# Kernel tuning notes

Hardware: AMD Instinct MI355X
Metric: run time of the kernel (lower is better)

The kernel has to match this reference:

```python
import jax, jax.numpy as jnp
import numpy as np
from jax import lax

DIM = 1024
H = 16          # num_heads
HD = DIM // H   # head dim (qk and v identical)
D_INNER = 4     # fast-weight inner dim
CHUNK = 16
BASE_LR = 1e-3
KSZ = 4         # short conv kernel size


def short_conv(x, w):
    # x: (b, l, c), w: (c, KSZ). Depthwise causal conv + residual (as in ShortConvolution).
    xT = jnp.transpose(x, (0, 2, 1))  # (b, c, l)
    y = lax.conv_general_dilated(xT, w[:, None, :], window_strides=(1,),
                                 padding=[(KSZ - 1, 0)], feature_group_count=x.shape[-1],
                                 dimension_numbers=('NCH', 'OIH', 'NCH'))
    return jnp.transpose(y + xT, (0, 2, 1))


def l2norm(x):
    # interpret torch.norm(..., dim=-1) as L2 normalization over head dim (required for shape consistency)
    return x / jnp.linalg.norm(x, axis=-1, keepdims=True)


def attn(q, k, v):
    # flash_attn_func equivalent: non-causal softmax attention, scale 1/sqrt(d)
    # q: (b, D, h, d), k/v: (b, L, h, d)
    s = jnp.einsum('bqhd,bkhd->bhqk', q, k) / jnp.sqrt(jnp.asarray(q.shape[-1], q.dtype))
    p = jax.nn.softmax(s, axis=-1)
    return jnp.einsum('bhqk,bkhd->bqhd', p, v)


def setup_inputs() -> dict:
    key = jax.random.key(0)
    ks = jax.random.split(key, 12)
    b, l = 4, 4096
    s = 1.0 / np.sqrt(DIM)
    return {
        'hidden_states': jax.random.normal(ks[0], (b, l, DIM), jnp.float32),
        'Wq': jax.random.normal(ks[1], (DIM, DIM), jnp.float32) * s,
        'Wk': jax.random.normal(ks[2], (DIM, DIM), jnp.float32) * s,
        'Wv': jax.random.normal(ks[3], (DIM, DIM), jnp.float32) * s,
        'Wlr': jax.random.normal(ks[4], (H * 2, DIM), jnp.float32) * s,
        'Wg': jax.random.normal(ks[5], (DIM, DIM), jnp.float32) * s,
        'Wo': jax.random.normal(ks[6], (DIM, DIM), jnp.float32) * s,
        'cq': jax.random.normal(ks[7], (DIM, KSZ), jnp.float32) * 0.1,
        'ck': jax.random.normal(ks[8], (DIM, KSZ), jnp.float32) * 0.1,
        'cv': jax.random.normal(ks[9], (DIM, KSZ), jnp.float32) * 0.1,
        'W_in_init': jax.random.normal(ks[10], (1, D_INNER, H, HD), jnp.float32) / np.sqrt(HD),
        'W_out_init': jax.random.normal(ks[11], (1, D_INNER, H, HD), jnp.float32) / np.sqrt(D_INNER),
        'ln_g': jnp.ones((HD,), jnp.float32),
        'ln_b': jnp.zeros((HD,), jnp.float32),
    }


def _forward(hidden_states, Wq, Wk, Wv, Wlr, Wg, Wo, cq, ck, cv, W_in_init, W_out_init, ln_g, ln_b):
    b, l, _ = hidden_states.shape
    q = l2norm(jax.nn.silu(short_conv(hidden_states @ Wq.T, cq)).reshape(b, l, H, HD))
    k = l2norm(jax.nn.silu(short_conv(hidden_states @ Wk.T, ck)).reshape(b, l, H, HD))
    v = jax.nn.silu(short_conv(hidden_states @ Wv.T, cv)).reshape(b, l, H, HD)
    lr = jax.nn.softplus(hidden_states @ Wlr.T + BASE_LR).reshape(b, l, H, 2)

    nc = l // CHUNK
    to_chunks = lambda x: x.reshape(b, nc, CHUNK, H, -1).transpose(1, 0, 2, 3, 4)
    qc, kc, vc, lrc = map(to_chunks, (q, k, v, lr))

    W_in0 = jnp.broadcast_to(W_in_init, (b, D_INNER, H, HD))
    W_out0 = jnp.broadcast_to(W_out_init, (b, D_INNER, H, HD))
    mask = jnp.tril(jnp.ones((CHUNK, CHUNK), jnp.float32))  # causal within chunk (diag kept)

    def step(carry, xs):
        W_in, W_out = carry
        q_t, k_t, v_t, lr_t = xs  # (b, CHUNK, H, d) / lr (b, CHUNK, H, 2)
        k_h = jax.nn.softmax(jnp.einsum('blhd,bDhd->blhD', k_t, W_in), axis=-1) * lr_t[..., 1:]
        q_h = jax.nn.softmax(jnp.einsum('blhd,bDhd->blhD', q_t, W_in), axis=-1)
        qk = jnp.einsum('bqhD,bkhD->bhqk', q_h, k_h) * mask
        o_t = jnp.einsum('bqhD,bDhd->bqhd', q_h, W_out) + jnp.einsum('bhqk,bkhd->bqhd', qk, v_t)
        W_out = W_out + jnp.einsum('bnhD,bnhd->bDhd', k_h, v_t)
        lr_in = lr_t[:, :1, :, 0:1]    # (b,1,h,1)
        lr_out = lr_t[:, :1, :, 1:2]
        # two nested test-time gradient steps via attention
        for _ in range(2):
            g_out = -attn(W_in, k_t, v_t)
            g_in = -attn(W_out, v_t, k_t)
            W_in = W_in - lr_in * g_in
            W_out = W_out - lr_out * g_out
        return (W_in, W_out), o_t

    _, o = lax.scan(step, (W_in0, W_out0), (qc, kc, vc, lrc))
    o = o.transpose(1, 0, 2, 3, 4).reshape(b, l, H, HD)

    mu = o.mean(-1, keepdims=True)
    var = ((o - mu) ** 2).mean(-1, keepdims=True)
    o = (o - mu) / jnp.sqrt(var + 1e-5) * ln_g + ln_b
    o = o.reshape(b, l, DIM)
    gate = hidden_states @ Wg.T
    return (o * gate) @ Wo.T


def reference(hidden_states, Wq, Wk, Wv, Wlr, Wg, Wo, cq, ck, cv, W_in_init, W_out_init, ln_g, ln_b):
    return _forward(hidden_states, Wq, Wk, Wv, Wlr, Wg, Wo, cq, ck, cv, W_in_init, W_out_init, ln_g, ln_b)
```

## Files before the change

### kernel.cpp

```cpp
#include <hip/hip_runtime.h>
#include <cstdint>
#include <cstddef>

#define DIM    1024
#define NH     16
#define HD     64
#define CHUNK_ 16
#define SEQ    4096
#define BATCH  4
#define NROWS  (BATCH * SEQ)
#define NCHUNK (SEQ / CHUNK_)
#define SEG    64
#define NSEG   (SEQ / SEG)

using bf16x8 = __attribute__((ext_vector_type(8))) short;
using f32x4  = __attribute__((ext_vector_type(4))) float;
typedef union { bf16x8 v; uint32_t u[4]; } B8;

#define MFMA16(a, b, c) __builtin_amdgcn_mfma_f32_16x16x32_bf16((a), (b), (c), 0, 0, 0)

__device__ __forceinline__ ushort f2bf(float f) {
    uint32_t u = __float_as_uint(f);
    u += 0x7FFFu + ((u >> 16) & 1u);
    return (ushort)(u >> 16);
}
__device__ __forceinline__ uint32_t pack2(float a, float b) {
    return (uint32_t)f2bf(a) | ((uint32_t)f2bf(b) << 16);
}
__device__ __forceinline__ float b2f(ushort u) {
    return __uint_as_float(((uint32_t)u) << 16);
}
__device__ __forceinline__ float dot4(const float4 a, const float4 b) {
    return a.x*b.x + a.y*b.y + a.z*b.z + a.w*b.w;
}

template <int N>
__device__ __forceinline__ float ror16(float x) {
    return __int_as_float(__builtin_amdgcn_update_dpp(
        0, __float_as_int(x), 0x120 + N, 0xF, 0xF, true));
}
__device__ __forceinline__ float dppsum16(float x) {
    x += ror16<1>(x); x += ror16<2>(x);
    x += ror16<4>(x); x += ror16<8>(x);
    return x;
}

#define SYNC() do { asm volatile("" ::: "memory");          \
                    __builtin_amdgcn_wave_barrier();        \
                    __builtin_amdgcn_sched_barrier(0); } while (0)

__device__ __forceinline__ void gl_lds16(const void* g, void* l) {
    __builtin_amdgcn_global_load_lds(
        (const __attribute__((address_space(1))) void*)g,
        (__attribute__((address_space(3))) void*)l, 16, 0, 0);
}

__global__ __launch_bounds__(256)
void f2b_kernel(const float* __restrict__ in, ushort* __restrict__ out, int n8)
{
    int i = blockIdx.x * 256 + threadIdx.x;
    const int stride = gridDim.x * 256;
    for (; i < n8; i += stride) {
        float4 a = *(const float4*)&in[(size_t)i * 8];
        float4 b = *(const float4*)&in[(size_t)i * 8 + 4];
        uint4 u;
        u.x = pack2(a.x, a.y); u.y = pack2(a.z, a.w);
        u.z = pack2(b.x, b.y); u.w = pack2(b.z, b.w);
        *(uint4*)&out[(size_t)i * 8] = u;
    }
}

#define GEMM_LDS_BODY(EPILOG)                                                  \
    __shared__ ushort As[128][64];                                             \
    __shared__ ushort Bs[128][64];                                             \
    const int tid  = threadIdx.x, wave = tid >> 6, lane = tid & 63;            \
    const int m0   = blockIdx.y * 128, n0 = blockIdx.x * 128;                  \
    const int lo   = lane & 15, kg = lane >> 4;                                \
    const int wm   = (wave >> 1) * 64, wn = (wave & 1) * 64;                   \
    const int rin  = lane >> 3, sl = lane & 7;                                 \
    const int sb   = 32 * wave;                                                \
    f32x4 acc[4][4];                                                           \
    _Pragma("unroll")                                                          \
    for (int i = 0; i < 4; ++i)                                                \
        _Pragma("unroll")                                                      \
        for (int j = 0; j < 4; ++j) acc[i][j] = (f32x4){0.f, 0.f, 0.f, 0.f};   \
    const int swz = lo & 7;                                                    \
    for (int kt = 0; kt < K; kt += 64) {                                       \
        __syncthreads();                                                       \
        _Pragma("unroll")                                                      \
        for (int i = 0; i < 4; ++i) {                                          \
            const int row = sb + 8 * i + rin;                                  \
            const int gs  = sl ^ (row & 7);                                    \
            gl_lds16(A + (size_t)(m0 + row) * K + kt + gs * 8,                 \
                     &As[sb + 8 * i][0]);                                      \
            gl_lds16(B + (size_t)(n0 + row) * K + kt + gs * 8,                 \
                     &Bs[sb + 8 * i][0]);                                      \
        }                                                                      \
        __syncthreads();                                                       \
        bf16x8 af[2][4], bfr[2][4];                                            \
        _Pragma("unroll")                                                      \
        for (int kk = 0; kk < 2; ++kk)                                         \
            _Pragma("unroll")                                                  \
            for (int m = 0; m < 4; ++m) {                                      \
                const int s = (kk * 4 + kg) ^ swz;                             \
                af[kk][m]  = *(const bf16x8*)&As[wm + m * 16 + lo][s * 8];     \
                bfr[kk][m] = *(const bf16x8*)&Bs[wn + m * 16 + lo][s * 8];     \
            }                                                                  \
        _Pragma("unroll")                                                      \
        for (int kk = 0; kk < 2; ++kk)                                         \
            _Pragma("unroll")                                                  \
            for (int mt = 0; mt < 4; ++mt)                                     \
                _Pragma("unroll")                                              \
                for (int nt = 0; nt < 4; ++nt)                                 \
                    acc[mt][nt] = MFMA16(af[kk][mt], bfr[kk][nt], acc[mt][nt]);\
    }                                                                          \
    const int col = lane & 15, r4 = (lane >> 4) * 4;                           \
    _Pragma("unroll")                                                          \
    for (int mt = 0; mt < 4; ++mt)                                             \
        _Pragma("unroll")                                                      \
        for (int nt = 0; nt < 4; ++nt)                                         \
            _Pragma("unroll")                                                  \
            for (int j = 0; j < 4; ++j) {                                      \
                size_t idx = (size_t)(m0 + wm + mt * 16 + r4 + j) * DIM +      \
                             n0 + wn + nt * 16 + col;                          \
                EPILOG;                                                        \
            }

__global__ __launch_bounds__(256)
void gemm_lds_b16o(const ushort* __restrict__ A, const ushort* __restrict__ B,
                   ushort* __restrict__ C, int K)
{
    GEMM_LDS_BODY(C[idx] = f2bf(acc[mt][nt][j]))
}

__global__ __launch_bounds__(256)
void gemm_lds_f32o(const ushort* __restrict__ A, const ushort* __restrict__ B,
                   float* __restrict__ C, int K)
{
    GEMM_LDS_BODY(C[idx] = acc[mt][nt][j])
}

__global__ __launch_bounds__(256)
void lr_kernel(const float* __restrict__ hs, const float* __restrict__ Wlr,
               float* __restrict__ LR)
{
    __shared__ float row[DIM];
    const int r = blockIdx.x;
    const int t = threadIdx.x;
    *(float4*)&row[t * 4] = *(const float4*)&hs[(size_t)r * DIM + t * 4];
    __syncthreads();

    const int o = t >> 3;
    const int p = t & 7;
    const float* w = Wlr + (size_t)o * DIM + p * 128;
    const float* x = row + p * 128;
    float acc = 0.f;
#pragma unroll
    for (int i = 0; i < 32; ++i) {
        float4 xv = *(const float4*)(x + i * 4);
        float4 wv = *(const float4*)(w + i * 4);
        acc += dot4(xv, wv);
    }
    acc += __shfl_xor(acc, 1);
    acc += __shfl_xor(acc, 2);
    acc += __shfl_xor(acc, 4);
    if (p == 0) {
        float xx = acc + 0.001f;
        LR[(size_t)r * 32 + o] = (xx > 20.f) ? xx : log1pf(expf(xx));
    }
}

__global__ __launch_bounds__(256)
void halo_save(const ushort* __restrict__ Q, const ushort* __restrict__ K,
               const ushort* __restrict__ V, ushort* __restrict__ HALO)
{
    int idx = blockIdx.x;
    int tn  = idx / (BATCH * (NSEG - 1) * 3);
    int rem = idx - tn * (BATCH * (NSEG - 1) * 3);
    int b   = rem / ((NSEG - 1) * 3);
    int rem2= rem - b * ((NSEG - 1) * 3);
    int s   = rem2 / 3 + 1;
    int j   = rem2 - (s - 1) * 3;

    const ushort* buf = (tn == 0) ? Q : ((tn == 1) ? K : V);
    size_t src = ((size_t)(b * SEQ + s * SEG - 3 + j)) * DIM + threadIdx.x * 4;
    size_t dst = ((size_t)((tn * BATCH + b) * NSEG + s) * 3 + j) * DIM + threadIdx.x * 4;
    *(uint2*)&HALO[dst] = *(const uint2*)&buf[src];
}

__global__ __launch_bounds__(256)
void conv_inplace(ushort* __restrict__ Q, ushort* __restrict__ K,
                  ushort* __restrict__ V, const ushort* __restrict__ HALO,
                  const float* __restrict__ cq, const float* __restrict__ ck,
                  const float* __restrict__ cv)
{
    const int wid  = (blockIdx.x << 2) + (threadIdx.x >> 6);
    const int lane = threadIdx.x & 63;
    const int tn   = wid >> 12;
    const int rem  = wid & 4095;
    const int b    = rem >> 10;
    const int rem2 = rem & 1023;
    const int h    = rem2 >> 6;
    const int s    = rem2 & 63;
    const int c    = (h << 6) + lane;

    ushort* buf = (tn == 0) ? Q : ((tn == 1) ? K : V);
    const float* cw = (tn == 0) ? cq : ((tn == 1) ? ck : cv);
    float4 w4 = *(const float4*)(cw + (c << 2));

    float xm3 = 0.f, xm2 = 0.f, xm1 = 0.f;
    if (s > 0) {
        size_t hb = ((size_t)((tn * BATCH + b) * NSEG + s) * 3) * DIM + c;
        xm3 = b2f(HALO[hb]);
        xm2 = b2f(HALO[hb + DIM]);
        xm1 = b2f(HALO[hb + 2 * DIM]);
    }

    size_t base = ((size_t)(b * SEQ + s * SEG)) * DIM + c;
    float x_next = b2f(buf[base]);
#pragma unroll 4
    for (int i = 0; i < SEG; ++i) {
        float x = x_next;
        if (i < SEG - 1) x_next = b2f(buf[base + (size_t)(i + 1) * DIM]);
        float y = xm3 * w4.x + xm2 * w4.y + xm1 * w4.z + x * w4.w + x;
        y = y / (1.f + __expf(-y));
        if (tn < 2) {
            float n2 = y * y;
#pragma unroll
            for (int m = 1; m < 64; m <<= 1) n2 += __shfl_xor(n2, m);
            y *= rsqrtf(n2);
        }
        buf[base + (size_t)i * DIM] = f2bf(y);
        xm3 = xm2; xm2 = xm1; xm1 = x;
    }
}

__global__ __launch_bounds__(64)
void scan_kernel(const ushort* QP, const ushort* __restrict__ KP,
                 const ushort* __restrict__ VP, const float* __restrict__ LRb,
                 const float* __restrict__ GATE,
                 const float* __restrict__ Wi0, const float* __restrict__ Wo0,
                 const float* __restrict__ lng, const float* __restrict__ lnb,
                 ushort* OB)
{
    const int bh = blockIdx.x, b = bh >> 4, h = bh & 15;
    const int t  = threadIdx.x, lo = t & 15, g = t >> 4;

    __shared__ ushort KA2[2][16][72], QA2[2][16][72], VA2[2][16][72];
    __shared__ float  sG2[2][16][68];
    __shared__ ushort KT2[2][64][24];
    __shared__ ushort VT2[2][64][40];
    __shared__ ushort WiA[16][72], WoA[16][72];
    __shared__ ushort QKT[16][32], KH[16][32];

    for (int i = t; i < 16 * 72; i += 64) { ((ushort*)WiA)[i] = 0; ((ushort*)WoA)[i] = 0; }
    for (int i = t; i < 2 * 64 * 24; i += 64) ((ushort*)KT2)[i] = 0;
    for (int i = t; i < 2 * 64 * 40; i += 64) ((ushort*)VT2)[i] = 0;
    for (int i = t; i < 16 * 32; i += 64) { ((ushort*)QKT)[i] = 0; ((ushort*)KH)[i] = 0; }

    f32x4 wiC[4], woC[4];
#pragma unroll
    for (int n = 0; n < 4; ++n) { wiC[n] = (f32x4){0,0,0,0}; woC[n] = (f32x4){0,0,0,0}; }
    if (g == 0) {
#pragma unroll
        for (int n = 0; n < 4; ++n)
#pragma unroll
            for (int D = 0; D < 4; ++D) {
                float wi = Wi0[((size_t)D * NH + h) * HD + 16 * n + lo];
                float wo = Wo0[((size_t)D * NH + h) * HD + 16 * n + lo];
                wiC[n][D] = wi; woC[n][D] = wo;
                WiA[D][16 * n + lo] = f2bf(wi);
                WoA[D][16 * n + lo] = f2bf(wo);
                VT2[0][16 * n + lo][16 + D] = f2bf(wo);
            }
    }
    SYNC();

    float lnGr[4], lnBr[4];
#pragma unroll
    for (int n = 0; n < 4; ++n) { lnGr[n] = lng[16 * n + lo]; lnBr[n] = lnb[16 * n + lo]; }

    const int rowb = b * SEQ;
    const ushort* QPh = QP + h * 64;
    const ushort* KPh = KP + h * 64;
    const ushort* VPh = VP + h * 64;
    const float*  GPh = GATE + h * 64;
    ushort*       OBh = OB + h * 64;

    uint2 pq[4], pk[4], pv[4];
    float4 pg[4];
    float plr_q, plr_i, plr_o;

    {
#pragma unroll
        for (int i = 0; i < 4; ++i) {
            size_t go = (size_t)(rowb + i * 4 + g) * DIM + 4 * lo;
            pq[i] = *(const uint2*)&QPh[go];
            pk[i] = *(const uint2*)&KPh[go];
            pv[i] = *(const uint2*)&VPh[go];
            pg[i] = *(const float4*)&GPh[go];
        }
        plr_q = LRb[(size_t)(rowb + lo) * 32 + h * 2 + 1];
        plr_i = LRb[(size_t)rowb * 32 + h * 2];
        plr_o = LRb[(size_t)rowb * 32 + h * 2 + 1];
    }

    auto STAGE = [&](int nb) {
#pragma unroll
        for (int i = 0; i < 4; ++i) {
            const int row = i * 4 + g;
            *(float4*)&sG2[nb][row][4 * lo] = pg[i];
            *(uint2*)&QA2[nb][row][4 * lo] = pq[i];
            *(uint2*)&KA2[nb][row][4 * lo] = pk[i];
            *(uint2*)&VA2[nb][row][4 * lo] = pv[i];
            uint2 uk = pk[i], uv = pv[i];
            KT2[nb][4 * lo + 0][row] = (ushort)(uk.x & 0xFFFF);
            KT2[nb][4 * lo + 1][row] = (ushort)(uk.x >> 16);
            KT2[nb][4 * lo + 2][row] = (ushort)(uk.y & 0xFFFF);
            KT2[nb][4 * lo + 3][row] = (ushort)(uk.y >> 16);
            VT2[nb][4 * lo + 0][row] = (ushort)(uv.x & 0xFFFF);
            VT2[nb][4 * lo + 1][row] = (ushort)(uv.x >> 16);
            VT2[nb][4 * lo + 2][row] = (ushort)(uv.y & 0xFFFF);
            VT2[nb][4 * lo + 3][row] = (ushort)(uv.y >> 16);
        }
    };

    STAGE(0);
    SYNC();

    const f32x4 z4 = (f32x4){0.f, 0.f, 0.f, 0.f};
    const uint32_t pmsk = (g < 2) ? 0xFFFFFFFFu : 0u;
    const int L0 = (lo + 32 * g) & 63, L1 = (L0 + 16) & 63;

    for (int c = 0; c < NCHUNK; ++c) {
        const int rb  = rowb + c * CHUNK_;
        const int cur = c & 1, nxt = cur ^ 1;
        ushort (*KAc)[72] = KA2[cur];
        ushort (*QAc)[72] = QA2[cur];
        ushort (*VAc)[72] = VA2[cur];
        float  (*sGc)[68] = sG2[cur];
        ushort (*KTc)[24] = KT2[cur];
        ushort (*VTc)[40] = VT2[cur];

        const float lr1    = plr_q;
        const float lr_in  = plr_i;
        const float lr_out = plr_o;

        if (c + 1 < NCHUNK) {
            const int rb2 = rb + CHUNK_;
#pragma unroll
            for (int i = 0; i < 4; ++i) {
                size_t go = (size_t)(rb2 + i * 4 + g) * DIM + 4 * lo;
                pq[i] = *(const uint2*)&QPh[go];
                pk[i] = *(const uint2*)&KPh[go];
                pv[i] = *(const uint2*)&VPh[go];
                pg[i] = *(const float4*)&GPh[go];
            }
            plr_q = LRb[(size_t)(rb2 + lo) * 32 + h * 2 + 1];
            plr_i = LRb[(size_t)rb2 * 32 + h * 2];
            plr_o = LRb[(size_t)rb2 * 32 + h * 2 + 1];
        }

        bf16x8 xWi0 = *(const bf16x8*)&WiA[lo][g * 8];
        bf16x8 xWi1 = *(const bf16x8*)&WiA[lo][g * 8 + 32];
        f32x4 cK = MFMA16(xWi0, *(const bf16x8*)&KAc[lo][g * 8], z4);
        cK = MFMA16(xWi1, *(const bf16x8*)&KAc[lo][g * 8 + 32], cK);
        f32x4 cQ = MFMA16(xWi0, *(const bf16x8*)&QAc[lo][g * 8], z4);
        cQ = MFMA16(xWi1, *(const bf16x8*)&QAc[lo][g * 8 + 32], cQ);

        float mK = fmaxf(fmaxf(cK[0], cK[1]), fmaxf(cK[2], cK[3]));
        float ek0 = __expf(cK[0] - mK), ek1 = __expf(cK[1] - mK);
        float ek2 = __expf(cK[2] - mK), ek3 = __expf(cK[3] - mK);
        float ivk = lr1 / (ek0 + ek1 + ek2 + ek3);
        float kh0 = ek0 * ivk, kh1 = ek1 * ivk, kh2 = ek2 * ivk, kh3 = ek3 * ivk;

        float mQ = fmaxf(fmaxf(cQ[0], cQ[1]), fmaxf(cQ[2], cQ[3]));
        float eq0 = __expf(cQ[0] - mQ), eq1 = __expf(cQ[1] - mQ);
        float eq2 = __expf(cQ[2] - mQ), eq3 = __expf(cQ[3] - mQ);
        float ivq = 1.f / (eq0 + eq1 + eq2 + eq3);
        float qh0 = eq0 * ivq, qh1 = eq1 * ivq, qh2 = eq2 * ivq, qh3 = eq3 * ivq;

        B8 aQh, bKh;
        aQh.u[0] = aQh.u[1] = aQh.u[2] = aQh.u[3] = 0;
        bKh.u[0] = bKh.u[1] = bKh.u[2] = bKh.u[3] = 0;
        if (g == 0) {
            aQh.u[0] = pack2(qh0, qh1); aQh.u[1] = pack2(qh2, qh3);
            bKh.u[0] = pack2(kh0, kh1); bKh.u[1] = pack2(kh2, kh3);
        }
        f32x4 cQK = MFMA16(aQh.v, bKh.v, z4);

#pragma unroll
        for (int r = 0; r < 4; ++r) {
            const int q = 4 * g + r;
            QKT[q][lo] = (lo <= q) ? f2bf(cQK[r]) : (ushort)0;
        }
        if (g == 0) {
            QKT[lo][16] = f2bf(qh0); QKT[lo][17] = f2bf(qh1);
            QKT[lo][18] = f2bf(qh2); QKT[lo][19] = f2bf(qh3);
            KH[0][lo] = f2bf(kh0); KH[1][lo] = f2bf(kh1);
            KH[2][lo] = f2bf(kh2); KH[3][lo] = f2bf(kh3);
        }
        SYNC();

        bf16x8 aO = *(const bf16x8*)&QKT[lo][g * 8];
        f32x4 oA[4];
#pragma unroll
        for (int n = 0; n < 4; ++n)
            oA[n] = MFMA16(aO, *(const bf16x8*)&VTc[16 * n + lo][g * 8], z4);
#pragma unroll
        for (int r = 0; r < 4; ++r) {
            float s1 = oA[0][r] + oA[1][r] + oA[2][r] + oA[3][r];
            float s2 = oA[0][r] * oA[0][r] + oA[1][r] * oA[1][r] +
                       oA[2][r] * oA[2][r] + oA[3][r] * oA[3][r];
            s1 = dppsum16(s1); s2 = dppsum16(s2);
            float mu = s1 * (1.f / 64.f);
            float rstd = rsqrtf(s2 * (1.f / 64.f) - mu * mu + 1e-5f);
            const int q = 4 * g + r;
#pragma unroll
            for (int n = 0; n < 4; ++n) {
                float val = (oA[n][r] - mu) * rstd * lnGr[n] + lnBr[n];
                val *= sGc[q][16 * n + lo];
                OBh[(size_t)(rb + q) * DIM + 16 * n + lo] = f2bf(val);
            }
        }
        {
            bf16x8 aKH = *(const bf16x8*)&KH[lo][g * 8];
#pragma unroll
            for (int n = 0; n < 4; ++n)
                woC[n] = MFMA16(aKH, *(const bf16x8*)&VTc[16 * n + lo][g * 8], woC[n]);
        }
        if (g == 0) {
#pragma unroll
            for (int n = 0; n < 4; ++n)
#pragma unroll
                for (int D = 0; D < 4; ++D)
                    WoA[D][16 * n + lo] = f2bf(woC[n][D]);
        }
        SYNC();

#pragma unroll
        for (int it = 0; it < 2; ++it) {
            bf16x8 aK0 = *(const bf16x8*)&KAc[lo][g * 8];
            bf16x8 aK1 = *(const bf16x8*)&KAc[lo][g * 8 + 32];
            bf16x8 aV0 = *(const bf16x8*)&VAc[lo][g * 8];
            bf16x8 aV1 = *(const bf16x8*)&VAc[lo][g * 8 + 32];
            bf16x8 bWi0 = *(const bf16x8*)&WiA[lo][g * 8];
            bf16x8 bWi1 = *(const bf16x8*)&WiA[lo][g * 8 + 32];
            bf16x8 bWo0 = *(const bf16x8*)&WoA[lo][g * 8];
            bf16x8 bWo1 = *(const bf16x8*)&WoA[lo][g * 8 + 32];
            f32x4 s0T = MFMA16(aK0, bWi0, z4);
            s0T = MFMA16(aK1, bWi1, s0T);
            f32x4 s1T = MFMA16(aV0, bWo0, z4);
            s1T = MFMA16(aV1, bWo1, s1T);

            float x0[4], x1[4];
#pragma unroll
            for (int r = 0; r < 4; ++r) {
                x0[r] = s0T[r] * 0.125f;
                x1[r] = s1T[r] * 0.125f;
            }
            float m0 = fmaxf(fmaxf(x0[0], x0[1]), fmaxf(x0[2], x0[3]));
            float m1 = fmaxf(fmaxf(x1[0], x1[1]), fmaxf(x1[2], x1[3]));
            m0 = fmaxf(m0, __shfl_xor(m0, 16)); m0 = fmaxf(m0, __shfl_xor(m0, 32));
            m1 = fmaxf(m1, __shfl_xor(m1, 16)); m1 = fmaxf(m1, __shfl_xor(m1, 32));
            float e0[4], e1[4];
#pragma unroll
            for (int r = 0; r < 4; ++r) {
                e0[r] = __expf(x0[r] - m0);
                e1[r] = __expf(x1[r] - m1);
            }
            float su0 = e0[0] + e0[1] + e0[2] + e0[3];
            float su1 = e1[0] + e1[1] + e1[2] + e1[3];
            su0 += __shfl_xor(su0, 16); su0 += __shfl_xor(su0, 32);
            su1 += __shfl_xor(su1, 16); su1 += __shfl_xor(su1, 32);
            const float w0 = lr_out / su0;
            const float w1 = lr_in / su1;

            uint32_t p00 = pack2(e0[0] * w0, e0[1] * w0);
            uint32_t p01 = pack2(e0[2] * w0, e0[3] * w0);
            uint32_t p10 = pack2(e1[0] * w1, e1[1] * w1);
            uint32_t p11 = pack2(e1[2] * w1, e1[3] * w1);
            B8 aP0, aP1;
            aP0.u[0] = (uint32_t)__shfl((int)p00, L0) & pmsk;
            aP0.u[1] = (uint32_t)__shfl((int)p01, L0) & pmsk;
            aP0.u[2] = (uint32_t)__shfl((int)p00, L1) & pmsk;
            aP0.u[3] = (uint32_t)__shfl((int)p01, L1) & pmsk;
            aP1.u[0] = (uint32_t)__shfl((int)p10, L0) & pmsk;
            aP1.u[1] = (uint32_t)__shfl((int)p11, L0) & pmsk;
            aP1.u[2] = (uint32_t)__shfl((int)p10, L1) & pmsk;
            aP1.u[3] = (uint32_t)__shfl((int)p11, L1) & pmsk;

#pragma unroll
            for (int n = 0; n < 4; ++n) {
                woC[n] = MFMA16(aP0.v, *(const bf16x8*)&VTc[16 * n + lo][g * 8], woC[n]);
                wiC[n] = MFMA16(aP1.v, *(const bf16x8*)&KTc[16 * n + lo][g * 8], wiC[n]);
            }

            if (it == 1 && c + 1 < NCHUNK) STAGE(nxt);

            if (g == 0) {
#pragma unroll
                for (int n = 0; n < 4; ++n)
#pragma unroll
                    for (int D = 0; D < 4; ++D) {
                        WiA[D][16 * n + lo] = f2bf(wiC[n][D]);
                        WoA[D][16 * n + lo] = f2bf(woC[n][D]);
                        if (it == 1) VT2[nxt][16 * n + lo][16 + D] = f2bf(woC[n][D]);
                    }
            }
            SYNC();
        }
    }
}

extern "C" void kernel_launch(void* const* d_in, const int* in_sizes, int n_in,
                              void* d_out, int out_size, void* d_ws, size_t ws_size,
                              hipStream_t stream)
{
    const float* hs  = (const float*)d_in[0];
    const float* Wq  = (const float*)d_in[1];
    const float* Wk  = (const float*)d_in[2];
    const float* Wv  = (const float*)d_in[3];
    const float* Wlr = (const float*)d_in[4];
    const float* Wg  = (const float*)d_in[5];
    const float* Wo  = (const float*)d_in[6];
    const float* cq  = (const float*)d_in[7];
    const float* ck  = (const float*)d_in[8];
    const float* cv  = (const float*)d_in[9];
    const float* Wi0 = (const float*)d_in[10];
    const float* Wo0 = (const float*)d_in[11];
    const float* lng = (const float*)d_in[12];
    const float* lnb = (const float*)d_in[13];

    ushort* Qb   = (ushort*)d_ws;
    ushort* Kb   = Qb + (size_t)NROWS * DIM;
    ushort* Vb   = Kb + (size_t)NROWS * DIM;
    ushort* hsb  = Vb + (size_t)NROWS * DIM;
    ushort* Wqb  = hsb + (size_t)NROWS * DIM;
    ushort* Wkb  = Wqb + (size_t)DIM * DIM;
    ushort* Wvb  = Wkb + (size_t)DIM * DIM;
    ushort* Wgb  = Wvb + (size_t)DIM * DIM;
    ushort* Wob  = Wgb + (size_t)DIM * DIM;
    ushort* HALO = Wob + (size_t)DIM * DIM;
    float*  LRb  = (float*)(HALO + (size_t)3 * BATCH * NSEG * 3 * DIM);
    float*  GATE = (float*)d_out;
    ushort* OBUF = hsb;

    dim3 blk(256);

    f2b_kernel<<<2048, blk, 0, stream>>>(hs, hsb, NROWS * DIM / 8);
    f2b_kernel<<<512, blk, 0, stream>>>(Wq, Wqb, DIM * DIM / 8);
    f2b_kernel<<<512, blk, 0, stream>>>(Wk, Wkb, DIM * DIM / 8);
    f2b_kernel<<<512, blk, 0, stream>>>(Wv, Wvb, DIM * DIM / 8);
    f2b_kernel<<<512, blk, 0, stream>>>(Wg, Wgb, DIM * DIM / 8);
    f2b_kernel<<<512, blk, 0, stream>>>(Wo, Wob, DIM * DIM / 8);

    gemm_lds_b16o<<<dim3(8, 128), blk, 0, stream>>>(hsb, Wqb, Qb, 1024);
    gemm_lds_b16o<<<dim3(8, 128), blk, 0, stream>>>(hsb, Wkb, Kb, 1024);
    gemm_lds_b16o<<<dim3(8, 128), blk, 0, stream>>>(hsb, Wvb, Vb, 1024);
    gemm_lds_f32o<<<dim3(8, 128), blk, 0, stream>>>(hsb, Wgb, GATE, 1024);

    lr_kernel<<<NROWS, blk, 0, stream>>>(hs, Wlr, LRb);

    halo_save<<<3 * BATCH * (NSEG - 1) * 3, blk, 0, stream>>>(Qb, Kb, Vb, HALO);
    conv_inplace<<<(3 * BATCH * NH * NSEG) / 4, blk, 0, stream>>>(Qb, Kb, Vb, HALO,
                                                                  cq, ck, cv);

    scan_kernel<<<BATCH * NH, dim3(64), 0, stream>>>(Qb, Kb, Vb, LRb, GATE,
                                                     Wi0, Wo0, lng, lnb, OBUF);

    gemm_lds_f32o<<<dim3(8, 128), blk, 0, stream>>>(OBUF, Wob, (float*)d_out, 1024);
}
```

Before: 1.751 ms.

## Keep fast-weight fragments in registers via shuffles and merge weight conversion launches

The scan kernel now holds the W_in/W_out fast-weight MFMA fragments in registers and rebuilds them with cross-lane shuffles, instead of writing them to shared memory and reading them back. This removes the WiA/WoA/KH LDS buffers, the k-hat LDS round trip and one barrier per chunk. It also reuses the transposed K-score MFMA from the forward step for the first gradient iteration. The five weight-conversion launches are merged into one kernel. The cost is more shuffles and more register pressure in a latency-bound serial scan running 64 single-wave blocks.

After: 1.796 ms. 2.6% more time.

```diff
diff --git a/kernel.cpp b/kernel.cpp
--- a/kernel.cpp
+++ b/kernel.cpp
@@ -67,6 +67,26 @@
         u.x = pack2(a.x, a.y); u.y = pack2(a.z, a.w);
         u.z = pack2(b.x, b.y); u.w = pack2(b.z, b.w);
         *(uint4*)&out[(size_t)i * 8] = u;
+    }
+}
+
+__global__ __launch_bounds__(256)
+void f2b5_kernel(const float* __restrict__ w0, const float* __restrict__ w1,
+                 const float* __restrict__ w2, const float* __restrict__ w3,
+                 const float* __restrict__ w4, ushort* __restrict__ out)
+{
+    const int W8 = DIM * DIM / 8;
+    const int w  = blockIdx.x >> 7;
+    const float* src = (w == 0) ? w0 : (w == 1) ? w1 : (w == 2) ? w2
+                     : (w == 3) ? w3 : w4;
+    ushort* dst = out + (size_t)w * DIM * DIM;
+    for (int i = (blockIdx.x & 127) * 256 + threadIdx.x; i < W8; i += 128 * 256) {
+        float4 a = *(const float4*)&src[(size_t)i * 8];
+        float4 b = *(const float4*)&src[(size_t)i * 8 + 4];
+        uint4 u;
+        u.x = pack2(a.x, a.y); u.y = pack2(a.z, a.w);
+        u.z = pack2(b.x, b.y); u.w = pack2(b.z, b.w);
+        *(uint4*)&dst[(size_t)i * 8] = u;
     }
 }
 
@@ -235,6 +255,35 @@
     }
 }
 
+#define BUILD_WFRAG(W, F0, F1) do {                                           \
+    uint32_t pa0 = pack2(W[0][0], W[0][1]), pb0 = pack2(W[0][2], W[0][3]);    \
+    uint32_t pa1 = pack2(W[1][0], W[1][1]), pb1 = pack2(W[1][2], W[1][3]);    \
+    uint32_t pa2 = pack2(W[2][0], W[2][1]), pb2 = pack2(W[2][2], W[2][3]);    \
+    uint32_t pa3 = pack2(W[3][0], W[3][1]), pb3 = pack2(W[3][2], W[3][3]);    \
+    uint32_t a0L0 = (uint32_t)__shfl((int)pa0, Lw0);                          \
+    uint32_t a1L0 = (uint32_t)__shfl((int)pa1, Lw0);                          \
+    uint32_t a2L0 = (uint32_t)__shfl((int)pa2, Lw0);                          \
+    uint32_t a3L0 = (uint32_t)__shfl((int)pa3, Lw0);                          \
+    uint32_t b0L0 = (uint32_t)__shfl((int)pb0, Lw0);                          \
+    uint32_t b1L0 = (uint32_t)__shfl((int)pb1, Lw0);                          \
+    uint32_t b2L0 = (uint32_t)__shfl((int)pb2, Lw0);                          \
+    uint32_t b3L0 = (uint32_t)__shfl((int)pb3, Lw0);                          \
+    uint32_t a0L1 = (uint32_t)__shfl((int)pa0, Lw1);                          \
+    uint32_t a1L1 = (uint32_t)__shfl((int)pa1, Lw1);                          \
+    uint32_t a2L1 = (uint32_t)__shfl((int)pa2, Lw1);                          \
+    uint32_t a3L1 = (uint32_t)__shfl((int)pa3, Lw1);                          \
+    uint32_t b0L1 = (uint32_t)__shfl((int)pb0, Lw1);                          \
+    uint32_t b1L1 = (uint32_t)__shfl((int)pb1, Lw1);                          \
+    uint32_t b2L1 = (uint32_t)__shfl((int)pb2, Lw1);                          \
+    uint32_t b3L1 = (uint32_t)__shfl((int)pb3, Lw1);                          \
+    B8 f0_, f1_;                                                              \
+    f0_.u[0] = selg ? a1L0 : a0L0;  f0_.u[1] = selg ? b1L0 : b0L0;            \
+    f0_.u[2] = selg ? a1L1 : a0L1;  f0_.u[3] = selg ? b1L1 : b0L1;            \
+    f1_.u[0] = selg ? a3L0 : a2L0;  f1_.u[1] = selg ? b3L0 : b2L0;            \
+    f1_.u[2] = selg ? a3L1 : a2L1;  f1_.u[3] = selg ? b3L1 : b2L1;            \
+    F0 = f0_.v; F1 = f1_.v;                                                   \
+} while (0)
+
 __global__ __launch_bounds__(64)
 void scan_kernel(const ushort* QP, const ushort* __restrict__ KP,
                  const ushort* __restrict__ VP, const float* __restrict__ LRb,
@@ -250,29 +299,31 @@
     __shared__ float  sG2[2][16][68];
     __shared__ ushort KT2[2][64][24];
     __shared__ ushort VT2[2][64][40];
-    __shared__ ushort WiA[16][72], WoA[16][72];
-    __shared__ ushort QKT[16][32], KH[16][32];
-
-    for (int i = t; i < 16 * 72; i += 64) { ((ushort*)WiA)[i] = 0; ((ushort*)WoA)[i] = 0; }
+    __shared__ ushort QKT[16][32];
+
     for (int i = t; i < 2 * 64 * 24; i += 64) ((ushort*)KT2)[i] = 0;
     for (int i = t; i < 2 * 64 * 40; i += 64) ((ushort*)VT2)[i] = 0;
-    for (int i = t; i < 16 * 32; i += 64) { ((ushort*)QKT)[i] = 0; ((ushort*)KH)[i] = 0; }
+    for (int i = t; i < 16 * 32; i += 64) ((ushort*)QKT)[i] = 0;
 
     f32x4 wiC[4], woC[4];
 #pragma unroll
-    for (int n = 0; n < 4; ++n) { wiC[n] = (f32x4){0,0,0,0}; woC[n] = (f32x4){0,0,0,0}; }
-    if (g == 0) {
+    for (int n = 0; n < 4; ++n)
+#pragma unroll
+        for (int r = 0; r < 4; ++r) {
+            const int d = 16 * n + 4 * g + r;
+            float wi = 0.f, wo = 0.f;
+            if (lo < 4) {
+                wi = Wi0[((size_t)lo * NH + h) * HD + d];
+                wo = Wo0[((size_t)lo * NH + h) * HD + d];
+            }
+            wiC[n][r] = wi; woC[n][r] = wo;
+        }
+    if (lo < 4) {
 #pragma unroll
         for (int n = 0; n < 4; ++n)
 #pragma unroll
-            for (int D = 0; D < 4; ++D) {
-                float wi = Wi0[((size_t)D * NH + h) * HD + 16 * n + lo];
-                float wo = Wo0[((size_t)D * NH + h) * HD + 16 * n + lo];
-                wiC[n][D] = wi; woC[n][D] = wo;
-                WiA[D][16 * n + lo] = f2bf(wi);
-                WoA[D][16 * n + lo] = f2bf(wo);
-                VT2[0][16 * n + lo][16 + D] = f2bf(wo);
-            }
+            for (int r = 0; r < 4; ++r)
+                VT2[0][16 * n + 4 * g + r][16 + lo] = f2bf(woC[n][r]);
     }
     SYNC();
 
@@ -290,7 +341,6 @@
     uint2 pq[4], pk[4], pv[4];
     float4 pg[4];
     float plr_q, plr_i, plr_o;
-
     {
 #pragma unroll
         for (int i = 0; i < 4; ++i) {
@@ -331,6 +381,11 @@
     const f32x4 z4 = (f32x4){0.f, 0.f, 0.f, 0.f};
     const uint32_t pmsk = (g < 2) ? 0xFFFFFFFFu : 0u;
     const int L0 = (lo + 32 * g) & 63, L1 = (L0 + 16) & 63;
+    const int Lw0 = lo + 32 * (g & 1), Lw1 = Lw0 + 16;
+    const int selg = g & 2;
+
+    bf16x8 fWi0, fWi1, fWo0, fWo1;
+    BUILD_WFRAG(wiC, fWi0, fWi1);
 
     for (int c = 0; c < NCHUNK; ++c) {
         const int rb  = rowb + c * CHUNK_;
@@ -342,7 +397,7 @@
         ushort (*KTc)[24] = KT2[cur];
         ushort (*VTc)[40] = VT2[cur];
 
-        const float lr1    = plr_q;
+        const float lr1v   = plr_q;
         const float lr_in  = plr_i;
         const float lr_out = plr_o;
 
@@ -361,17 +416,21 @@
             plr_o = LRb[(size_t)rb2 * 32 + h * 2 + 1];
         }
 
-        bf16x8 xWi0 = *(const bf16x8*)&WiA[lo][g * 8];
-        bf16x8 xWi1 = *(const bf16x8*)&WiA[lo][g * 8 + 32];
-        f32x4 cK = MFMA16(xWi0, *(const bf16x8*)&KAc[lo][g * 8], z4);
-        cK = MFMA16(xWi1, *(const bf16x8*)&KAc[lo][g * 8 + 32], cK);
-        f32x4 cQ = MFMA16(xWi0, *(const bf16x8*)&QAc[lo][g * 8], z4);
-        cQ = MFMA16(xWi1, *(const bf16x8*)&QAc[lo][g * 8 + 32], cQ);
+        bf16x8 aKA0 = *(const bf16x8*)&KAc[lo][g * 8];
+        bf16x8 aKA1 = *(const bf16x8*)&KAc[lo][g * 8 + 32];
+        bf16x8 aQA0 = *(const bf16x8*)&QAc[lo][g * 8];
+        bf16x8 aQA1 = *(const bf16x8*)&QAc[lo][g * 8 + 32];
+        bf16x8 aVA0 = *(const bf16x8*)&VAc[lo][g * 8];
+        bf16x8 aVA1 = *(const bf16x8*)&VAc[lo][g * 8 + 32];
+
+        f32x4 cK = MFMA16(fWi0, aKA0, z4);  cK = MFMA16(fWi1, aKA1, cK);
+        f32x4 cQ = MFMA16(fWi0, aQA0, z4);  cQ = MFMA16(fWi1, aQA1, cQ);
+        f32x4 cKT = MFMA16(aKA0, fWi0, z4); cKT = MFMA16(aKA1, fWi1, cKT);
 
         float mK = fmaxf(fmaxf(cK[0], cK[1]), fmaxf(cK[2], cK[3]));
         float ek0 = __expf(cK[0] - mK), ek1 = __expf(cK[1] - mK);
         float ek2 = __expf(cK[2] - mK), ek3 = __expf(cK[3] - mK);
-        float ivk = lr1 / (ek0 + ek1 + ek2 + ek3);
+        float ivk = lr1v / (ek0 + ek1 + ek2 + ek3);
         float kh0 = ek0 * ivk, kh1 = ek1 * ivk, kh2 = ek2 * ivk, kh3 = ek3 * ivk;
 
         float mQ = fmaxf(fmaxf(cQ[0], cQ[1]), fmaxf(cQ[2], cQ[3]));
@@ -379,6 +438,25 @@
         float eq2 = __expf(cQ[2] - mQ), eq3 = __expf(cQ[3] - mQ);
         float ivq = 1.f / (eq0 + eq1 + eq2 + eq3);
         float qh0 = eq0 * ivq, qh1 = eq1 * ivq, qh2 = eq2 * ivq, qh3 = eq3 * ivq;
+
+        float khT[4];
+#pragma unroll
+        for (int r = 0; r < 4; ++r) {
+            float v = cKT[r];
+            float m = fmaxf(v, __shfl_xor(v, 1));
+            m = fmaxf(m, __shfl_xor(m, 2));
+            float e = __expf(v - m);
+            float s = e + __shfl_xor(e, 1);
+            s += __shfl_xor(s, 2);
+            khT[r] = e / s * __shfl(lr1v, 4 * g + r);
+        }
+        uint32_t kpkA = pack2(khT[0], khT[1]);
+        uint32_t kpkB = pack2(khT[2], khT[3]);
+        B8 Ykh;
+        Ykh.u[0] = (uint32_t)__shfl((int)kpkA, L0) & pmsk;
+        Ykh.u[1] = (uint32_t)__shfl((int)kpkB, L0) & pmsk;
+        Ykh.u[2] = (uint32_t)__shfl((int)kpkA, L1) & pmsk;
+        Ykh.u[3] = (uint32_t)__shfl((int)kpkB, L1) & pmsk;
 
         B8 aQh, bKh;
         aQh.u[0] = aQh.u[1] = aQh.u[2] = aQh.u[3] = 0;
@@ -397,16 +475,20 @@
         if (g == 0) {
             QKT[lo][16] = f2bf(qh0); QKT[lo][17] = f2bf(qh1);
             QKT[lo][18] = f2bf(qh2); QKT[lo][19] = f2bf(qh3);
-            KH[0][lo] = f2bf(kh0); KH[1][lo] = f2bf(kh1);
-            KH[2][lo] = f2bf(kh2); KH[3][lo] = f2bf(kh3);
         }
         SYNC();
 
         bf16x8 aO = *(const bf16x8*)&QKT[lo][g * 8];
+        bf16x8 vfr[4], kfr[4];
+#pragma unroll
+        for (int n = 0; n < 4; ++n) {
+            vfr[n] = *(const bf16x8*)&VTc[16 * n + lo][g * 8];
+            kfr[n] = *(const bf16x8*)&KTc[16 * n + lo][g * 8];
+        }
         f32x4 oA[4];
 #pragma unroll
         for (int n = 0; n < 4; ++n)
-            oA[n] = MFMA16(aO, *(const bf16x8*)&VTc[16 * n + lo][g * 8], z4);
+            oA[n] = MFMA16(aO, vfr[n], z4);
 #pragma unroll
         for (int r = 0; r < 4; ++r) {
             float s1 = oA[0][r] + oA[1][r] + oA[2][r] + oA[3][r];
@@ -423,35 +505,22 @@
                 OBh[(size_t)(rb + q) * DIM + 16 * n + lo] = f2bf(val);
             }
         }
-        {
-            bf16x8 aKH = *(const bf16x8*)&KH[lo][g * 8];
-#pragma unroll
-            for (int n = 0; n < 4; ++n)
-                woC[n] = MFMA16(aKH, *(const bf16x8*)&VTc[16 * n + lo][g * 8], woC[n]);
-        }
-        if (g == 0) {
-#pragma unroll
-            for (int n = 0; n < 4; ++n)
-#pragma unroll
-                for (int D = 0; D < 4; ++D)
-                    WoA[D][16 * n + lo] = f2bf(woC[n][D]);
-        }
-        SYNC();
+#pragma unroll
+        for (int n = 0; n < 4; ++n)
+            woC[n] = MFMA16(vfr[n], Ykh.v, woC[n]);
+        BUILD_WFRAG(woC, fWo0, fWo1);
 
 #pragma unroll
         for (int it = 0; it < 2; ++it) {
-            bf16x8 aK0 = *(const bf16x8*)&KAc[lo][g * 8];
-            bf16x8 aK1 = *(const bf16x8*)&KAc[lo][g * 8 + 32];
-            bf16x8 aV0 = *(const bf16x8*)&VAc[lo][g * 8];
-            bf16x8 aV1 = *(const bf16x8*)&VAc[lo][g * 8 + 32];
-            bf16x8 bWi0 = *(const bf16x8*)&WiA[lo][g * 8];
-            bf16x8 bWi1 = *(const bf16x8*)&WiA[lo][g * 8 + 32];
-            bf16x8 bWo0 = *(const bf16x8*)&WoA[lo][g * 8];
-            bf16x8 bWo1 = *(const bf16x8*)&WoA[lo][g * 8 + 32];
-            f32x4 s0T = MFMA16(aK0, bWi0, z4);
-            s0T = MFMA16(aK1, bWi1, s0T);
-            f32x4 s1T = MFMA16(aV0, bWo0, z4);
-            s1T = MFMA16(aV1, bWo1, s1T);
+            f32x4 s0T;
+            if (it == 0) {
+                s0T = cKT;
+            } else {
+                s0T = MFMA16(aKA0, fWi0, z4);
+                s0T = MFMA16(aKA1, fWi1, s0T);
+            }
+            f32x4 s1T = MFMA16(aVA0, fWo0, z4);
+            s1T = MFMA16(aVA1, fWo1, s1T);
 
             float x0[4], x1[4];
 #pragma unroll
@@ -492,21 +561,21 @@
 
 #pragma unroll
             for (int n = 0; n < 4; ++n) {
-                woC[n] = MFMA16(aP0.v, *(const bf16x8*)&VTc[16 * n + lo][g * 8], woC[n]);
-                wiC[n] = MFMA16(aP1.v, *(const bf16x8*)&KTc[16 * n + lo][g * 8], wiC[n]);
-            }
-
-            if (it == 1 && c + 1 < NCHUNK) STAGE(nxt);
-
-            if (g == 0) {
-#pragma unroll
-                for (int n = 0; n < 4; ++n)
-#pragma unroll
-                    for (int D = 0; D < 4; ++D) {
-                        WiA[D][16 * n + lo] = f2bf(wiC[n][D]);
-                        WoA[D][16 * n + lo] = f2bf(woC[n][D]);
-                        if (it == 1) VT2[nxt][16 * n + lo][16 + D] = f2bf(woC[n][D]);
-                    }
+                woC[n] = MFMA16(vfr[n], aP0.v, woC[n]);
+                wiC[n] = MFMA16(kfr[n], aP1.v, wiC[n]);
+            }
+            BUILD_WFRAG(wiC, fWi0, fWi1);
+            BUILD_WFRAG(woC, fWo0, fWo1);
+
+            if (it == 1 && c + 1 < NCHUNK) {
+                if (lo < 4) {
+#pragma unroll
+                    for (int n = 0; n < 4; ++n)
+#pragma unroll
+                        for (int r = 0; r < 4; ++r)
+                            VT2[nxt][16 * n + 4 * g + r][16 + lo] = f2bf(woC[n][r]);
+                }
+                STAGE(nxt);
             }
             SYNC();
         }
@@ -549,11 +618,7 @@
     dim3 blk(256);
 
     f2b_kernel<<<2048, blk, 0, stream>>>(hs, hsb, NROWS * DIM / 8);
-    f2b_kernel<<<512, blk, 0, stream>>>(Wq, Wqb, DIM * DIM / 8);
-    f2b_kernel<<<512, blk, 0, stream>>>(Wk, Wkb, DIM * DIM / 8);
-    f2b_kernel<<<512, blk, 0, stream>>>(Wv, Wvb, DIM * DIM / 8);
-    f2b_kernel<<<512, blk, 0, stream>>>(Wg, Wgb, DIM * DIM / 8);
-    f2b_kernel<<<512, blk, 0, stream>>>(Wo, Wob, DIM * DIM / 8);
+    f2b5_kernel<<<640, blk, 0, stream>>>(Wq, Wk, Wv, Wg, Wo, Wqb);
 
     gemm_lds_b16o<<<dim3(8, 128), blk, 0, stream>>>(hsb, Wqb, Qb, 1024);
     gemm_lds_b16o<<<dim3(8, 128), blk, 0, stream>>>(hsb, Wkb, Kb, 1024);
```
